# Kernel tuning notes

Hardware: AMD Instinct MI355X
Metric: run time of the kernel (lower is better)

Reference implementation:

```python
import jax, jax.numpy as jnp
import numpy as np

B, S, K, N = 4, 2048, 1024, 4096


def setup_inputs() -> dict:
    key = jax.random.key(0)
    k1, k2, k3, k4, k5 = jax.random.split(key, 5)
    # int8 activations/weights as produced by static affine quantization (zero_point_domain=NONE)
    x_int8 = jax.random.randint(k1, (B, S, K), -128, 128, dtype=jnp.int32).astype(jnp.int8)
    w_int8 = jax.random.randint(k2, (N, K), -128, 128, dtype=jnp.int32).astype(jnp.int8)
    scale_i = jax.random.uniform(k3, (), minval=0.01, maxval=0.05, dtype=jnp.float32)   # per-tensor act scale
    scale_w = jax.random.uniform(k4, (N,), minval=0.001, maxval=0.01, dtype=jnp.float32)  # per-channel weight scale
    bias = jax.random.normal(k5, (N,), dtype=jnp.float32)
    return {"x_int8": x_int8, "w_int8": w_int8, "scale_i": scale_i, "scale_w": scale_w, "bias": bias}


def q(x, dtype):
    # denormal-flushing cast from the source; for float32 it is a plain cast
    # (module.weight.dtype == float32 here), kept as a helper for fidelity.
    if dtype == jnp.float16:
        return jnp.where(jnp.abs(x) < 2.0 ** -14, jnp.zeros_like(x), x).astype(jnp.float16)
    if dtype == jnp.bfloat16:
        return jnp.where(jnp.abs(x) < 2.0 ** -126, jnp.zeros_like(x), x).astype(jnp.bfloat16)
    return x.astype(dtype)


def reference(x_int8, w_int8, scale_i, scale_w, bias):
    # 'quantized'-mode forward of QModule wrapping a Linear:
    #   x = q(round(F.linear(x.double(), w.double())), dtype) * q(q(scale_i*scale_w, f32), f32)
    #   x = x + bias
    # round(double matmul of int8 values) is exact integer accumulation, so an
    # int32 GEMM is bit-identical (|acc| <= 127*127*1024 << 2^53 and < 2^31).
    acc = jnp.einsum('bsk,nk->bsn', x_int8.astype(jnp.int32), w_int8.astype(jnp.int32))  # [B,S,N] int32
    scale = q(q(scale_i * scale_w, jnp.float32), jnp.float32)  # [N]
    out = q(acc, jnp.float32) * scale + bias  # fused dequant/rescale + bias epilogue
    return out
```

## Files before the change

### kernel.cpp

```cpp
#include <hip/hip_runtime.h>
#include <stdint.h>

#define M_DIM 8192
#define N_DIM 4096
#define K_DIM 1024
#define BK    128

using i32x4 = __attribute__((ext_vector_type(4))) int;

__global__ __launch_bounds__(256) void pack_both(const int* __restrict__ X32,
                                                 const int* __restrict__ W32,
                                                 int* __restrict__ Xp,
                                                 int* __restrict__ Wp) {
    int b = blockIdx.x;
    const int4* s4;
    int4* d4;
    int u;
    if (b < 2048) {
        u  = b * 256 + threadIdx.x;
        s4 = (const int4*)X32;
        d4 = (int4*)Xp;
    } else {
        u  = (b - 2048) * 256 + threadIdx.x;
        s4 = (const int4*)W32;
        d4 = (int4*)Wp;
    }
    int4 o;
    #pragma unroll
    for (int i = 0; i < 4; ++i) {
        int4 v = s4[u * 4 + i];
        ((int*)&o)[i] = (v.x & 0xFF) | ((v.y & 0xFF) << 8) |
                        ((v.z & 0xFF) << 16) | (v.w << 24);
    }
    d4[u] = o;
}

__device__ __forceinline__ void cp16_async(const void* g, void* l) {
    __builtin_amdgcn_global_load_lds(
        (const __attribute__((address_space(1))) void*)g,
        (__attribute__((address_space(3))) void*)l,
        16, 0, 0);
}

__global__ __launch_bounds__(256, 2) void i8gemm_dequant(
    const int8_t* __restrict__ X,
    const int8_t* __restrict__ W,
    const float*  __restrict__ scale_i,
    const float*  __restrict__ scale_w,
    const float*  __restrict__ bias,
    float*        __restrict__ out)
{
    __shared__ int8_t lA[128 * BK];
    __shared__ int8_t lB[128 * BK];

    const int t     = threadIdx.x;
    const int lane  = t & 63;
    const int wave  = t >> 6;
    const int waveM = wave >> 1;
    const int waveN = wave & 1;

    const int bm = blockIdx.y * 128;
    const int bn = blockIdx.x * 128;

    i32x4 acc[4][4] = {};

    const int8_t* Asrc[4];
    const int8_t* Bsrc[4];
    int8_t* dA[4];
    int8_t* dB[4];
    #pragma unroll
    for (int s = 0; s < 4; ++s) {
        int c   = t + 256 * s;
        int row = c >> 3;
        int q   = (c & 7) ^ (row & 7);
        Asrc[s] = X + (size_t)(bm + row) * K_DIM + q * 16;
        Bsrc[s] = W + (size_t)(bn + row) * K_DIM + q * 16;
        dA[s]   = lA + (256 * s + wave * 64) * 16;
        dB[s]   = lB + (256 * s + wave * 64) * 16;
    }

    int aoff[2][4], boff[2][4];
    #pragma unroll
    for (int h = 0; h < 2; ++h) {
        #pragma unroll
        for (int i = 0; i < 4; ++i) {
            int r = waveM * 64 + i * 16 + (lane & 15);
            int q = (h * 4 + (lane >> 4)) ^ (r & 7);
            aoff[h][i] = r * BK + q * 16;
        }
        #pragma unroll
        for (int j = 0; j < 4; ++j) {
            int r = waveN * 64 + j * 16 + (lane & 15);
            int q = (h * 4 + (lane >> 4)) ^ (r & 7);
            boff[h][j] = r * BK + q * 16;
        }
    }

    for (int k0 = 0; k0 < K_DIM; k0 += BK) {
        #pragma unroll
        for (int s = 0; s < 4; ++s) {
            cp16_async(Asrc[s] + k0, dA[s]);
            cp16_async(Bsrc[s] + k0, dB[s]);
        }
        __syncthreads();

        i32x4 af[2][4], bf[2][4];
        #pragma unroll
        for (int h = 0; h < 2; ++h) {
            #pragma unroll
            for (int i = 0; i < 4; ++i) af[h][i] = *(const i32x4*)(lA + aoff[h][i]);
            #pragma unroll
            for (int j = 0; j < 4; ++j) bf[h][j] = *(const i32x4*)(lB + boff[h][j]);
        }

        #pragma unroll
        for (int h = 0; h < 2; ++h)
            #pragma unroll
            for (int i = 0; i < 4; ++i)
                #pragma unroll
                for (int j = 0; j < 4; ++j)
                    acc[i][j] = __builtin_amdgcn_mfma_i32_16x16x64_i8(
                        af[h][i], bf[h][j], acc[i][j], 0, 0, 0);

        __syncthreads();
    }

    const float si = scale_i[0];
    float s[4], b[4];
    int   ncol[4];
    #pragma unroll
    for (int j = 0; j < 4; ++j) {
        ncol[j] = bn + waveN * 64 + j * 16 + (lane & 15);
        s[j] = si * scale_w[ncol[j]];
        b[j] = bias[ncol[j]];
    }
    #pragma unroll
    for (int i = 0; i < 4; ++i) {
        int mbase = bm + waveM * 64 + i * 16 + ((lane >> 4) * 4);
        #pragma unroll
        for (int r = 0; r < 4; ++r) {
            size_t rowoff = (size_t)(mbase + r) * N_DIM;
            #pragma unroll
            for (int j = 0; j < 4; ++j) {
                out[rowoff + ncol[j]] = (float)acc[i][j][r] * s[j] + b[j];
            }
        }
    }
}

extern "C" void kernel_launch(void* const* d_in, const int* in_sizes, int n_in,
                              void* d_out, int out_size, void* d_ws, size_t ws_size,
                              hipStream_t stream) {
    const int* x32 = (const int*)d_in[0];
    const int* w32 = (const int*)d_in[1];
    const float* si = (const float*)d_in[2];
    const float* sw = (const float*)d_in[3];
    const float* bs = (const float*)d_in[4];
    float* out = (float*)d_out;

    int8_t* Xp = (int8_t*)d_ws;
    int8_t* Wp = (int8_t*)d_ws + (size_t)M_DIM * K_DIM;

    pack_both<<<3072, 256, 0, stream>>>(x32, w32, (int*)Xp, (int*)Wp);

    dim3 grid(N_DIM / 128, M_DIM / 128);
    i8gemm_dequant<<<grid, 256, 0, stream>>>(Xp, Wp, si, sw, bs, out);
}
```

Baseline: 196.3 us.

## Use 256x256 tiles with double-buffered LDS pipeline and XCD-aware block mapping

```diff
diff --git a/kernel.cpp b/kernel.cpp
--- a/kernel.cpp
+++ b/kernel.cpp
@@ -5,6 +5,7 @@
 #define N_DIM 4096
 #define K_DIM 1024
 #define BK    128
+#define NT    (K_DIM / BK)
 
 using i32x4 = __attribute__((ext_vector_type(4))) int;
 
@@ -42,7 +43,7 @@
         16, 0, 0);
 }
 
-__global__ __launch_bounds__(256, 2) void i8gemm_dequant(
+__global__ __launch_bounds__(512, 2) void i8gemm_dequant(
     const int8_t* __restrict__ X,
     const int8_t* __restrict__ W,
     const float*  __restrict__ scale_i,
@@ -50,99 +51,122 @@
     const float*  __restrict__ bias,
     float*        __restrict__ out)
 {
-    __shared__ int8_t lA[128 * BK];
-    __shared__ int8_t lB[128 * BK];
+    __shared__ int8_t lds[2][2][256 * BK];
 
     const int t     = threadIdx.x;
     const int lane  = t & 63;
     const int wave  = t >> 6;
-    const int waveM = wave >> 1;
-    const int waveN = wave & 1;
+    const int waveM = wave >> 2;
+    const int waveN = wave & 3;
 
-    const int bm = blockIdx.y * 128;
-    const int bn = blockIdx.x * 128;
+    const int bid = blockIdx.x;
+    const int xcd = bid & 7;
+    const int idx = bid >> 3;
+    const int bm  = ((xcd >> 1) * 8 + (idx >> 3)) * 256;
+    const int bn  = ((xcd & 1) * 8 + (idx & 7)) * 256;
 
-    i32x4 acc[4][4] = {};
-
-    const int8_t* Asrc[4];
-    const int8_t* Bsrc[4];
-    int8_t* dA[4];
-    int8_t* dB[4];
+    uint32_t Aoff[4], Boff[4];
+    int dL[4];
     #pragma unroll
     for (int s = 0; s < 4; ++s) {
-        int c   = t + 256 * s;
+        int c   = s * 512 + t;
         int row = c >> 3;
         int q   = (c & 7) ^ (row & 7);
-        Asrc[s] = X + (size_t)(bm + row) * K_DIM + q * 16;
-        Bsrc[s] = W + (size_t)(bn + row) * K_DIM + q * 16;
-        dA[s]   = lA + (256 * s + wave * 64) * 16;
-        dB[s]   = lB + (256 * s + wave * 64) * 16;
+        Aoff[s] = (uint32_t)(bm + row) * K_DIM + q * 16;
+        Boff[s] = (uint32_t)(bn + row) * K_DIM + q * 16;
+        dL[s]   = (s * 512 + wave * 64) * 16;
     }
 
-    int aoff[2][4], boff[2][4];
+    int aoff[8], boff[4];
     #pragma unroll
-    for (int h = 0; h < 2; ++h) {
-        #pragma unroll
-        for (int i = 0; i < 4; ++i) {
-            int r = waveM * 64 + i * 16 + (lane & 15);
-            int q = (h * 4 + (lane >> 4)) ^ (r & 7);
-            aoff[h][i] = r * BK + q * 16;
-        }
-        #pragma unroll
-        for (int j = 0; j < 4; ++j) {
-            int r = waveN * 64 + j * 16 + (lane & 15);
-            int q = (h * 4 + (lane >> 4)) ^ (r & 7);
-            boff[h][j] = r * BK + q * 16;
-        }
+    for (int i = 0; i < 8; ++i) {
+        int r = waveM * 128 + i * 16 + (lane & 15);
+        aoff[i] = r * BK + (((lane >> 4) ^ (r & 7)) * 16);
+    }
+    #pragma unroll
+    for (int j = 0; j < 4; ++j) {
+        int r = waveN * 64 + j * 16 + (lane & 15);
+        boff[j] = r * BK + (((lane >> 4) ^ (r & 7)) * 16);
     }
 
-    for (int k0 = 0; k0 < K_DIM; k0 += BK) {
-        #pragma unroll
-        for (int s = 0; s < 4; ++s) {
-            cp16_async(Asrc[s] + k0, dA[s]);
-            cp16_async(Bsrc[s] + k0, dB[s]);
-        }
-        __syncthreads();
+    i32x4 acc[8][4] = {};
 
-        i32x4 af[2][4], bf[2][4];
-        #pragma unroll
-        for (int h = 0; h < 2; ++h) {
-            #pragma unroll
-            for (int i = 0; i < 4; ++i) af[h][i] = *(const i32x4*)(lA + aoff[h][i]);
-            #pragma unroll
-            for (int j = 0; j < 4; ++j) bf[h][j] = *(const i32x4*)(lB + boff[h][j]);
-        }
+#define STAGE(b, tt)                                                      \
+    {                                                                     \
+        _Pragma("unroll") for (int s = 0; s < 4; ++s)                     \
+            cp16_async(X + Aoff[s] + (tt) * BK, &lds[b][0][dL[s]]);       \
+        _Pragma("unroll") for (int s = 0; s < 4; ++s)                     \
+            cp16_async(W + Boff[s] + (tt) * BK, &lds[b][1][dL[s]]);       \
+    }
 
-        #pragma unroll
-        for (int h = 0; h < 2; ++h)
-            #pragma unroll
-            for (int i = 0; i < 4; ++i)
-                #pragma unroll
-                for (int j = 0; j < 4; ++j)
-                    acc[i][j] = __builtin_amdgcn_mfma_i32_16x16x64_i8(
-                        af[h][i], bf[h][j], acc[i][j], 0, 0, 0);
+    STAGE(0, 0)
+    STAGE(1, 1)
+    asm volatile("s_waitcnt vmcnt(8)" ::: "memory");
+    __builtin_amdgcn_s_barrier();
 
-        __syncthreads();
+#define TILE_STEP(b, tt)                                                  \
+    {                                                                     \
+        const int8_t* pA = &lds[b][0][0];                                 \
+        const int8_t* pB = &lds[b][1][0];                                 \
+        i32x4 af[8], bf[4];                                               \
+        _Pragma("unroll") for (int i = 0; i < 8; ++i)                     \
+            af[i] = *(const i32x4*)(pA + aoff[i]);                        \
+        _Pragma("unroll") for (int j = 0; j < 4; ++j)                     \
+            bf[j] = *(const i32x4*)(pB + boff[j]);                        \
+        __builtin_amdgcn_s_setprio(1);                                    \
+        _Pragma("unroll") for (int i = 0; i < 8; ++i)                     \
+            _Pragma("unroll") for (int j = 0; j < 4; ++j)                 \
+                acc[i][j] = __builtin_amdgcn_mfma_i32_16x16x64_i8(        \
+                    af[i], bf[j], acc[i][j], 0, 0, 0);                    \
+        __builtin_amdgcn_s_setprio(0);                                    \
+        _Pragma("unroll") for (int i = 0; i < 8; ++i)                     \
+            af[i] = *(const i32x4*)(pA + (aoff[i] ^ 64));                 \
+        _Pragma("unroll") for (int j = 0; j < 4; ++j)                     \
+            bf[j] = *(const i32x4*)(pB + (boff[j] ^ 64));                 \
+        asm volatile("s_waitcnt lgkmcnt(0)" ::: "memory");                \
+        __builtin_amdgcn_s_barrier();                                     \
+        if ((tt) + 2 < NT) {                                              \
+            STAGE(b, (tt) + 2)                                            \
+            __builtin_amdgcn_sched_barrier(0);                            \
+        }                                                                 \
+        __builtin_amdgcn_s_setprio(1);                                    \
+        _Pragma("unroll") for (int i = 0; i < 8; ++i)                     \
+            _Pragma("unroll") for (int j = 0; j < 4; ++j)                 \
+                acc[i][j] = __builtin_amdgcn_mfma_i32_16x16x64_i8(        \
+                    af[i], bf[j], acc[i][j], 0, 0, 0);                    \
+        __builtin_amdgcn_s_setprio(0);                                    \
+        if ((tt) + 2 < NT) {                                              \
+            asm volatile("s_waitcnt vmcnt(8)" ::: "memory");              \
+        } else if ((tt) + 1 < NT) {                                       \
+            asm volatile("s_waitcnt vmcnt(0)" ::: "memory");              \
+        }                                                                 \
+        if ((tt) + 1 < NT) __builtin_amdgcn_s_barrier();                  \
+    }
+
+    #pragma unroll
+    for (int tp = 0; tp < NT; tp += 2) {
+        TILE_STEP(0, tp)
+        TILE_STEP(1, tp + 1)
     }
 
     const float si = scale_i[0];
-    float s[4], b[4];
+    float sc[4], bi[4];
     int   ncol[4];
     #pragma unroll
     for (int j = 0; j < 4; ++j) {
         ncol[j] = bn + waveN * 64 + j * 16 + (lane & 15);
-        s[j] = si * scale_w[ncol[j]];
-        b[j] = bias[ncol[j]];
+        sc[j] = si * scale_w[ncol[j]];
+        bi[j] = bias[ncol[j]];
     }
     #pragma unroll
-    for (int i = 0; i < 4; ++i) {
-        int mbase = bm + waveM * 64 + i * 16 + ((lane >> 4) * 4);
+    for (int i = 0; i < 8; ++i) {
+        int mbase = bm + waveM * 128 + i * 16 + ((lane >> 4) * 4);
         #pragma unroll
         for (int r = 0; r < 4; ++r) {
             size_t rowoff = (size_t)(mbase + r) * N_DIM;
             #pragma unroll
             for (int j = 0; j < 4; ++j) {
-                out[rowoff + ncol[j]] = (float)acc[i][j][r] * s[j] + b[j];
+                out[rowoff + ncol[j]] = (float)acc[i][j][r] * sc[j] + bi[j];
             }
         }
     }
@@ -163,6 +187,5 @@
 
     pack_both<<<3072, 256, 0, stream>>>(x32, w32, (int*)Xp, (int*)Wp);
 
-    dim3 grid(N_DIM / 128, M_DIM / 128);
-    i8gemm_dequant<<<grid, 256, 0, stream>>>(Xp, Wp, si, sw, bs, out);
+    i8gemm_dequant<<<dim3(512), dim3(512), 0, stream>>>(Xp, Wp, si, sw, bs, out);
 }
```

New measurement: 201.8 us. +2.8%, slower.
